# Performance work log

Measured on AMD Instinct MI355X. Metric: run time of the kernel, lower is better.

The kernel has to match this reference:

```python
import jax, jax.numpy as jnp
import numpy as np

B, S, H = 2, 2048, 1024
E, I, IS, K = 16, 512, 2048, 4


def setup_inputs() -> dict:
    key = jax.random.key(0)
    ks = jax.random.split(key, 8)
    s = 0.02
    return {
        "hidden_states": jax.random.normal(ks[0], (B, S, H), jnp.float32),
        "router_w": jax.random.normal(ks[1], (E, H), jnp.float32) * s,
        "gate_up_proj": jax.random.normal(ks[2], (E, 2 * I, H), jnp.float32) * s,
        "down_proj": jax.random.normal(ks[3], (E, H, I), jnp.float32) * s,
        "shared_gate_w": jax.random.normal(ks[4], (IS, H), jnp.float32) * s,
        "shared_up_w": jax.random.normal(ks[5], (IS, H), jnp.float32) * s,
        "shared_down_w": jax.random.normal(ks[6], (H, IS), jnp.float32) * s,
        "shared_expert_gate_w": jax.random.normal(ks[7], (1, H), jnp.float32) * s,
        "top_k": K,
    }


def reference(hidden_states, router_w, gate_up_proj, down_proj,
              shared_gate_w, shared_up_w, shared_down_w,
              shared_expert_gate_w, top_k):
    b, s, h_dim = hidden_states.shape
    N = b * s
    num_experts = router_w.shape[0]
    h = hidden_states.reshape(N, h_dim)

    # ---- shared expert (SwiGLU MLP) ----
    shared_out = (jax.nn.silu(h @ shared_gate_w.T) * (h @ shared_up_w.T)) @ shared_down_w.T
    shared_out = jax.nn.sigmoid(h @ shared_expert_gate_w.T) * shared_out  # [N, H]

    # ---- router: softmax -> top-k -> renormalize ----
    router_logits = h @ router_w.T  # [N, E]
    router_probs_f32 = jax.nn.softmax(router_logits.astype(jnp.float32), axis=-1)
    top_v, top_i = jax.lax.top_k(router_probs_f32, top_k)  # [N, K]
    top_v = top_v / jnp.sum(top_v, axis=-1, keepdims=True)
    top_v = top_v.astype(router_logits.dtype)

    # combine weights scattered to dense [N, E] (zero for unselected experts)
    one_hot = jax.nn.one_hot(top_i, num_experts, dtype=top_v.dtype)  # [N, K, E]
    combine = jnp.sum(one_hot * top_v[..., None], axis=1)  # [N, E]

    # ---- experts: dense dispatch, masked combine (same math as gather/scatter loop) ----
    gu = jnp.einsum('nh,eih->nei', h, gate_up_proj)  # [N, E, 2I]
    gate, up = jnp.split(gu, 2, axis=-1)
    act = jax.nn.silu(gate) * up  # [N, E, I]
    expert_out = jnp.einsum('nei,ehi,ne->nh', act, down_proj, combine)  # [N, H]

    out = expert_out + shared_out

    # ---- aux load-balancing loss (faithful to source, including its reductions) ----
    tokens_per_expert = jnp.sum(one_hot.astype(jnp.float32), axis=(0, 1))  # [E]
    fraction_tokens = tokens_per_expert / (N * top_k)
    router_probs_sum = jnp.sum(jax.nn.softmax(router_logits, axis=-1), axis=0)  # [E]
    fraction_probs = jnp.sum(router_probs_sum) / N  # scalar (as in source)
    aux_loss = num_experts * jnp.sum(fraction_tokens * fraction_probs)

    return out.reshape(b, s, h_dim), aux_loss
```

## Files before the change

### kernel.cpp

```cpp
#include <hip/hip_runtime.h>

typedef __bf16 bf16_t;
typedef bf16_t bf16x4v __attribute__((ext_vector_type(4)));
typedef bf16_t bf16x8v __attribute__((ext_vector_type(8)));
typedef float f32x4 __attribute__((ext_vector_type(4)));

__device__ __forceinline__ void gl_lds16(const void* g, void* l) {
  __builtin_amdgcn_global_load_lds((__attribute__((address_space(1))) void*)g,
                                   (__attribute__((address_space(3))) void*)l,
                                   16, 0, 0);
}

__device__ __forceinline__ float fast_silu(float x) {
  return x / (1.f + __expf(-x));
}

__global__ void cvt_f32_bf16_kernel(const float* __restrict__ in,
                                    bf16_t* __restrict__ out, int n4) {
  int i = blockIdx.x * blockDim.x + threadIdx.x;
  const int stride = gridDim.x * blockDim.x;
  const float4* in4 = (const float4*)in;
  bf16x4v* out4 = (bf16x4v*)out;
  for (; i < n4; i += stride) {
    float4 v = in4[i];
    bf16x4v o;
    o[0] = (bf16_t)v.x; o[1] = (bf16_t)v.y; o[2] = (bf16_t)v.z; o[3] = (bf16_t)v.w;
    out4[i] = o;
  }
}

__global__ __launch_bounds__(256)
void router_topk_kernel(const float* __restrict__ h, const float* __restrict__ rw,
                        const float* __restrict__ segw, float* __restrict__ gsig,
                        int* __restrict__ tokTopI, float* __restrict__ tokTopW) {
  const int t = threadIdx.x;
  const int lane = t & 63;
  const int wid = t >> 6;
  const int grp = lane >> 4;
  const int e = lane & 15;
  const int tok = blockIdx.x * 16 + wid * 4 + grp;

  const float4* h4 = (const float4*)(h + (size_t)tok * 1024);
  const float4* rw4 = (const float4*)(rw + (size_t)e * 1024);
  const float4* sg4 = (const float4*)segw;

  float s = 0.f, ss = 0.f;
  #pragma unroll 8
  for (int c = 0; c < 256; ++c) {
    float4 hv = h4[c];
    float4 wv = rw4[c];
    s += hv.x * wv.x + hv.y * wv.y + hv.z * wv.z + hv.w * wv.w;
    if ((c & 15) == e) {
      float4 gv = sg4[c];
      ss += hv.x * gv.x + hv.y * gv.y + hv.z * gv.z + hv.w * gv.w;
    }
  }
  #pragma unroll
  for (int m = 1; m <= 8; m <<= 1) ss += __shfl_xor(ss, m);
  float mx = s;
  #pragma unroll
  for (int m = 1; m <= 8; m <<= 1) mx = fmaxf(mx, __shfl_xor(mx, m));
  float p = expf(s - mx);

  float pc = p;
  float tsum = 0.f;
  float myw = 0.f; int myi = 0;
  #pragma unroll
  for (int r = 0; r < 4; ++r) {
    float v = pc; int idx = e;
    #pragma unroll
    for (int m = 1; m <= 8; m <<= 1) {
      float ov = __shfl_xor(v, m); int oi = __shfl_xor(idx, m);
      if (ov > v || (ov == v && oi < idx)) { v = ov; idx = oi; }
    }
    tsum += v;
    if (e == r) { myi = idx; myw = v; }
    if (e == idx) pc = -1.f;
  }
  if (e < 4) {
    tokTopI[tok * 4 + e] = myi;
    tokTopW[tok * 4 + e] = myw / tsum;
  }
  if (e == 0) gsig[tok] = 1.f / (1.f + expf(-ss));
}

__global__ __launch_bounds__(256)
void build_lists_kernel(const int* __restrict__ tokTopI,
                        const float* __restrict__ tokTopW,
                        int* __restrict__ cnt, int* __restrict__ toklist,
                        float* __restrict__ wlist) {
  const int e = blockIdx.x;
  const int t = threadIdx.x;
  const int lane = t & 63;
  const int wid = t >> 6;
  __shared__ int base;
  __shared__ int wsum[4];
  if (t == 0) base = 0;
  __syncthreads();

  for (int chunk = 0; chunk < 16; ++chunk) {
    const int i0 = chunk * 1024 + t * 4;
    int4 ti = *(const int4*)&tokTopI[i0];
    const bool f0 = ti.x == e, f1 = ti.y == e, f2 = ti.z == e, f3 = ti.w == e;
    const int c = (int)f0 + (int)f1 + (int)f2 + (int)f3;
    int inc = c;
    #pragma unroll
    for (int m = 1; m <= 32; m <<= 1) {
      int o = __shfl_up(inc, m);
      if (lane >= m) inc += o;
    }
    const int lanePre = inc - c;
    if (lane == 63) wsum[wid] = inc;
    __syncthreads();
    int wavePre = 0;
    #pragma unroll
    for (int w = 0; w < 4; ++w) if (w < wid) wavePre += wsum[w];
    const int total = wsum[0] + wsum[1] + wsum[2] + wsum[3];
    int pos = base + wavePre + lanePre;
    __syncthreads();
    if (t == 0) base += total;
    float4 tw = *(const float4*)&tokTopW[i0];
    if (f0) { toklist[e * 4096 + pos] = i0 >> 2;       wlist[e * 4096 + pos] = tw.x; pos++; }
    if (f1) { toklist[e * 4096 + pos] = (i0 + 1) >> 2; wlist[e * 4096 + pos] = tw.y; pos++; }
    if (f2) { toklist[e * 4096 + pos] = (i0 + 2) >> 2; wlist[e * 4096 + pos] = tw.z; pos++; }
    if (f3) { toklist[e * 4096 + pos] = (i0 + 3) >> 2; wlist[e * 4096 + pos] = tw.w; pos++; }
  }
  __syncthreads();
  if (t == 0) cnt[e] = base;
}

__global__ void finalize_router_kernel(const int* __restrict__ cnt,
                                       int* __restrict__ baseOff,
                                       float* __restrict__ aux) {
  if (threadIdx.x == 0 && blockIdx.x == 0) {
    int s = 0;
    for (int e = 0; e < 16; ++e) { baseOff[e] = s; s += cnt[e]; }
    aux[0] = 16.0f;
  }
}

template<bool GATHER>
__global__ __launch_bounds__(256, 2)
void gateup_gemm_kernel(const bf16_t* __restrict__ A,
                        const bf16_t* __restrict__ B1,
                        const bf16_t* __restrict__ B2,
                        size_t strideBe,
                        bf16_t* __restrict__ actOut, int ldAct,
                        int K, int Mfixed,
                        const int* __restrict__ cnt,
                        const int* __restrict__ baseOff,
                        const int* __restrict__ toklist) {
  const int e = blockIdx.z;
  const int rowBlk = blockIdx.y, colBlk = blockIdx.x;
  int M, actRowBase;
  if constexpr (GATHER) {
    M = cnt[e];
    if (rowBlk * 128 >= M) return;
    actRowBase = baseOff[e] + rowBlk * 128;
  } else {
    M = Mfixed;
    actRowBase = rowBlk * 128;
  }
  const bf16_t* b1 = B1 + (size_t)e * strideBe;
  const bf16_t* b2 = B2 + (size_t)e * strideBe;

  __shared__ __align__(16) bf16_t As[128 * 64];
  __shared__ __align__(16) bf16_t Bs[128 * 64];

  const int t = threadIdx.x;

  const bf16_t* aSrc[4];
  const bf16_t* bSrc[4];
  #pragma unroll
  for (int i = 0; i < 4; ++i) {
    int r = (t >> 3) + 32 * i;
    int grow;
    if constexpr (GATHER) {
      int rr = rowBlk * 128 + r;
      grow = (rr < M) ? toklist[e * 4096 + rr] : 0;
    } else {
      grow = rowBlk * 128 + r;
    }
    aSrc[i] = A + (size_t)grow * K + (t & 7) * 8;
    int j = colBlk * 64 + (r >> 1);
    bSrc[i] = ((r & 1) ? b2 : b1) + (size_t)j * K + (t & 7) * 8;
  }

  f32x4 acc[4][4];
  #pragma unroll
  for (int a = 0; a < 4; ++a)
    #pragma unroll
    for (int b = 0; b < 4; ++b)
      acc[a][b] = (f32x4){0.f, 0.f, 0.f, 0.f};

  const int lane = t & 63;
  const int wid = t >> 6;
  const int wm = wid >> 1, wn = wid & 1;
  const int lr = lane & 15;
  const int lk = (lane >> 4) * 8;

  bf16_t* aDst = As + t * 8;
  bf16_t* bDst = Bs + t * 8;

  for (int k0 = 0; k0 < K; k0 += 64) {
    #pragma unroll
    for (int i = 0; i < 4; ++i) gl_lds16(aSrc[i], aDst + i * 2048);
    #pragma unroll
    for (int i = 0; i < 4; ++i) gl_lds16(bSrc[i], bDst + i * 2048);
    #pragma unroll
    for (int i = 0; i < 4; ++i) { aSrc[i] += 64; bSrc[i] += 64; }
    __syncthreads();
    #pragma unroll
    for (int kk = 0; kk < 64; kk += 32) {
      bf16x8v af[4], bfr[4];
      #pragma unroll
      for (int f = 0; f < 4; ++f)
        af[f] = *(const bf16x8v*)&As[(wm * 64 + f * 16 + lr) * 64 + kk + lk];
      #pragma unroll
      for (int f = 0; f < 4; ++f)
        bfr[f] = *(const bf16x8v*)&Bs[(wn * 64 + f * 16 + lr) * 64 + kk + lk];
      #pragma unroll
      for (int fm = 0; fm < 4; ++fm)
        #pragma unroll
        for (int fn = 0; fn < 4; ++fn)
          acc[fm][fn] = __builtin_amdgcn_mfma_f32_16x16x32_bf16(
              af[fm], bfr[fn], acc[fm][fn], 0, 0, 0);
    }
    __syncthreads();
  }

  const int mRem = M - rowBlk * 128;
  #pragma unroll
  for (int fm = 0; fm < 4; ++fm) {
    #pragma unroll
    for (int fn = 0; fn < 4; ++fn) {
      const int nloc = wn * 64 + fn * 16 + lr;
      const int j = colBlk * 64 + (nloc >> 1);
      const bool even = (nloc & 1) == 0;
      #pragma unroll
      for (int r = 0; r < 4; ++r) {
        float mine = acc[fm][fn][r];
        float other = __shfl_xor(mine, 1);
        float gate = even ? mine : other;
        float up = even ? other : mine;
        float act = fast_silu(gate) * up;
        int tr = wm * 64 + fm * 16 + (lane >> 4) * 4 + r;
        if (even && tr < mRem)
          actOut[(size_t)(actRowBase + tr) * ldAct + j] = (bf16_t)act;
      }
    }
  }
}

template<bool EXPERT>
__global__ __launch_bounds__(256, 2)
void down_gemm_kernel(const bf16_t* __restrict__ Abase,
                      const bf16_t* __restrict__ Bbase,
                      size_t strideBe,
                      float* __restrict__ out,
                      const float* __restrict__ gsig,
                      int K, int Mfixed,
                      const int* __restrict__ cnt,
                      const int* __restrict__ baseOff,
                      const int* __restrict__ toklist,
                      const float* __restrict__ wlist) {
  const int e = blockIdx.z;
  const int rowBlk = blockIdx.y, colBlk = blockIdx.x;
  int M;
  const bf16_t* A;
  if constexpr (EXPERT) {
    M = cnt[e];
    if (rowBlk * 128 >= M) return;
    A = Abase + (size_t)baseOff[e] * K;
  } else {
    M = Mfixed;
    A = Abase;
  }
  const bf16_t* B = Bbase + (size_t)e * strideBe;

  __shared__ __align__(16) bf16_t As[128 * 64];
  __shared__ __align__(16) bf16_t Bs[128 * 64];

  const int t = threadIdx.x;
  const bf16_t* aSrc[4];
  const bf16_t* bSrc[4];
  #pragma unroll
  for (int i = 0; i < 4; ++i) {
    int r = (t >> 3) + 32 * i;
    aSrc[i] = A + (size_t)(rowBlk * 128 + r) * K + (t & 7) * 8;
    bSrc[i] = B + (size_t)(colBlk * 128 + r) * K + (t & 7) * 8;
  }

  f32x4 acc[4][4];
  #pragma unroll
  for (int a = 0; a < 4; ++a)
    #pragma unroll
    for (int b = 0; b < 4; ++b)
      acc[a][b] = (f32x4){0.f, 0.f, 0.f, 0.f};

  const int lane = t & 63;
  const int wid = t >> 6;
  const int wm = wid >> 1, wn = wid & 1;
  const int lr = lane & 15;
  const int lk = (lane >> 4) * 8;

  bf16_t* aDst = As + t * 8;
  bf16_t* bDst = Bs + t * 8;

  for (int k0 = 0; k0 < K; k0 += 64) {
    #pragma unroll
    for (int i = 0; i < 4; ++i) gl_lds16(aSrc[i], aDst + i * 2048);
    #pragma unroll
    for (int i = 0; i < 4; ++i) gl_lds16(bSrc[i], bDst + i * 2048);
    #pragma unroll
    for (int i = 0; i < 4; ++i) { aSrc[i] += 64; bSrc[i] += 64; }
    __syncthreads();
    #pragma unroll
    for (int kk = 0; kk < 64; kk += 32) {
      bf16x8v af[4], bfr[4];
      #pragma unroll
      for (int f = 0; f < 4; ++f)
        af[f] = *(const bf16x8v*)&As[(wm * 64 + f * 16 + lr) * 64 + kk + lk];
      #pragma unroll
      for (int f = 0; f < 4; ++f)
        bfr[f] = *(const bf16x8v*)&Bs[(wn * 64 + f * 16 + lr) * 64 + kk + lk];
      #pragma unroll
      for (int fm = 0; fm < 4; ++fm)
        #pragma unroll
        for (int fn = 0; fn < 4; ++fn)
          acc[fm][fn] = __builtin_amdgcn_mfma_f32_16x16x32_bf16(
              af[fm], bfr[fn], acc[fm][fn], 0, 0, 0);
    }
    __syncthreads();
  }

  const int mRem = M - rowBlk * 128;
  #pragma unroll
  for (int fm = 0; fm < 4; ++fm) {
    #pragma unroll
    for (int r = 0; r < 4; ++r) {
      const int tr = wm * 64 + fm * 16 + (lane >> 4) * 4 + r;
      if (tr < mRem) {
        int tok; float wgt;
        if constexpr (EXPERT) {
          int slot = e * 4096 + rowBlk * 128 + tr;
          tok = toklist[slot];
          wgt = wlist[slot];
        } else {
          tok = rowBlk * 128 + tr;
          wgt = gsig[tok];
        }
        float* orow = out + (size_t)tok * 1024;
        #pragma unroll
        for (int fn = 0; fn < 4; ++fn) {
          const int col = colBlk * 128 + wn * 64 + fn * 16 + lr;
          float v = acc[fm][fn][r] * wgt;
          if constexpr (EXPERT) atomicAdd(orow + col, v);
          else orow[col] = v;
        }
      }
    }
  }
}


extern "C" void kernel_launch(void* const* d_in, const int* in_sizes, int n_in,
                              void* d_out, int out_size, void* d_ws, size_t ws_size,
                              hipStream_t stream) {
  const float* h_f32 = (const float*)d_in[0];
  const float* rw    = (const float*)d_in[1];
  const float* gup   = (const float*)d_in[2];
  const float* dwn   = (const float*)d_in[3];
  const float* sgate = (const float*)d_in[4];
  const float* sup   = (const float*)d_in[5];
  const float* sdown = (const float*)d_in[6];
  const float* segw  = (const float*)d_in[7];

  char* ws = (char*)d_ws;
  bf16_t* h_bf    = (bf16_t*)(ws + 0);
  bf16_t* gup_bf  = (bf16_t*)(ws + 8388608);
  bf16_t* dwn_bf  = (bf16_t*)(ws + 41943040);
  bf16_t* sg_bf   = (bf16_t*)(ws + 58720256);
  bf16_t* su_bf   = (bf16_t*)(ws + 62914560);
  bf16_t* sd_bf   = (bf16_t*)(ws + 67108864);
  bf16_t* act_s   = (bf16_t*)(ws + 71303168);
  bf16_t* act_e   = (bf16_t*)(ws + 88080384);
  float*  gsig    = (float*)(ws + 105119744);
  int*    cnt     = (int*)(ws + 105136128);
  int*    baseOff = (int*)(ws + 105136384);
  int*    toklist = (int*)(ws + 105136640);
  float*  wlist   = (float*)(ws + 105398784);
  int*    tokTopI = (int*)(ws + 105660928);
  float*  tokTopW = (float*)(ws + 105726464);

  float* out = (float*)d_out;
  float* aux = out + 4194304;

  auto cvtLaunch = [&](const float* src, bf16_t* dst, int n) {
    int n4 = n / 4;
    int blocks = (n4 + 255) / 256;
    if (blocks > 2048) blocks = 2048;
    cvt_f32_bf16_kernel<<<blocks, 256, 0, stream>>>(src, dst, n4);
  };
  cvtLaunch(h_f32, h_bf, 4194304);
  cvtLaunch(gup,   gup_bf, 16777216);
  cvtLaunch(dwn,   dwn_bf, 8388608);
  cvtLaunch(sgate, sg_bf, 2097152);
  cvtLaunch(sup,   su_bf, 2097152);
  cvtLaunch(sdown, sd_bf, 2097152);

  router_topk_kernel<<<256, 256, 0, stream>>>(h_f32, rw, segw, gsig, tokTopI, tokTopW);
  build_lists_kernel<<<16, 256, 0, stream>>>(tokTopI, tokTopW, cnt, toklist, wlist);
  finalize_router_kernel<<<1, 64, 0, stream>>>(cnt, baseOff, aux);

  gateup_gemm_kernel<false><<<dim3(32, 32, 1), 256, 0, stream>>>(
      h_bf, sg_bf, su_bf, (size_t)0, act_s, 2048, 1024, 4096,
      nullptr, nullptr, nullptr);
  gateup_gemm_kernel<true><<<dim3(8, 32, 16), 256, 0, stream>>>(
      h_bf, gup_bf, gup_bf + 512 * 1024, (size_t)1024 * 1024, act_e, 512, 1024, 0,
      cnt, baseOff, toklist);
  down_gemm_kernel<false><<<dim3(8, 32, 1), 256, 0, stream>>>(
      act_s, sd_bf, (size_t)0, out, gsig, 2048, 4096,
      nullptr, nullptr, nullptr, nullptr);
  down_gemm_kernel<true><<<dim3(8, 32, 16), 256, 0, stream>>>(
      act_e, dwn_bf, (size_t)1024 * 512, out, nullptr, 512, 0,
      cnt, baseOff, toklist, wlist);
}
```

Before: 509.0 us.

## Replace expert atomic scatter with bf16 staging and combine kernel; swizzle LDS

The expert down-projection now writes weighted results as bf16 rows into a contiguous staging buffer instead of doing fp32 atomicAdd scatter into the output. A new combine kernel then gathers each token's four expert rows through a position map and adds them to the shared-expert output. Both GEMM kernels also XOR-swizzle their LDS tile layout to avoid bank conflicts, and launch bounds now request four blocks per SM. This removes atomic contention, but it adds an extra kernel pass, rounds expert partial outputs to bf16, and reuses the converted gate_up weight buffer as scratch after the gate/up GEMM has finished.

```diff
diff --git a/kernel.cpp b/kernel.cpp
--- a/kernel.cpp
+++ b/kernel.cpp
@@ -88,7 +88,7 @@
 void build_lists_kernel(const int* __restrict__ tokTopI,
                         const float* __restrict__ tokTopW,
                         int* __restrict__ cnt, int* __restrict__ toklist,
-                        float* __restrict__ wlist) {
+                        float* __restrict__ wlist, int* __restrict__ posOf) {
   const int e = blockIdx.x;
   const int t = threadIdx.x;
   const int lane = t & 63;
@@ -120,10 +120,10 @@
     __syncthreads();
     if (t == 0) base += total;
     float4 tw = *(const float4*)&tokTopW[i0];
-    if (f0) { toklist[e * 4096 + pos] = i0 >> 2;       wlist[e * 4096 + pos] = tw.x; pos++; }
-    if (f1) { toklist[e * 4096 + pos] = (i0 + 1) >> 2; wlist[e * 4096 + pos] = tw.y; pos++; }
-    if (f2) { toklist[e * 4096 + pos] = (i0 + 2) >> 2; wlist[e * 4096 + pos] = tw.z; pos++; }
-    if (f3) { toklist[e * 4096 + pos] = (i0 + 3) >> 2; wlist[e * 4096 + pos] = tw.w; pos++; }
+    if (f0) { toklist[e * 4096 + pos] = i0 >> 2;       wlist[e * 4096 + pos] = tw.x; posOf[i0]     = pos; pos++; }
+    if (f1) { toklist[e * 4096 + pos] = (i0 + 1) >> 2; wlist[e * 4096 + pos] = tw.y; posOf[i0 + 1] = pos; pos++; }
+    if (f2) { toklist[e * 4096 + pos] = (i0 + 2) >> 2; wlist[e * 4096 + pos] = tw.z; posOf[i0 + 2] = pos; pos++; }
+    if (f3) { toklist[e * 4096 + pos] = (i0 + 3) >> 2; wlist[e * 4096 + pos] = tw.w; posOf[i0 + 3] = pos; pos++; }
   }
   __syncthreads();
   if (t == 0) cnt[e] = base;
@@ -140,7 +140,7 @@
 }
 
 template<bool GATHER>
-__global__ __launch_bounds__(256, 2)
+__global__ __launch_bounds__(256, 4)
 void gateup_gemm_kernel(const bf16_t* __restrict__ A,
                         const bf16_t* __restrict__ B1,
                         const bf16_t* __restrict__ B2,
@@ -168,6 +168,7 @@
   __shared__ __align__(16) bf16_t Bs[128 * 64];
 
   const int t = threadIdx.x;
+  const int sc = (((t & 7) ^ ((t >> 3) & 7))) * 8;
 
   const bf16_t* aSrc[4];
   const bf16_t* bSrc[4];
@@ -181,9 +182,9 @@
     } else {
       grow = rowBlk * 128 + r;
     }
-    aSrc[i] = A + (size_t)grow * K + (t & 7) * 8;
+    aSrc[i] = A + (size_t)grow * K + sc;
     int j = colBlk * 64 + (r >> 1);
-    bSrc[i] = ((r & 1) ? b2 : b1) + (size_t)j * K + (t & 7) * 8;
+    bSrc[i] = ((r & 1) ? b2 : b1) + (size_t)j * K + sc;
   }
 
   f32x4 acc[4][4];
@@ -214,11 +215,15 @@
     for (int kk = 0; kk < 64; kk += 32) {
       bf16x8v af[4], bfr[4];
       #pragma unroll
-      for (int f = 0; f < 4; ++f)
-        af[f] = *(const bf16x8v*)&As[(wm * 64 + f * 16 + lr) * 64 + kk + lk];
-      #pragma unroll
-      for (int f = 0; f < 4; ++f)
-        bfr[f] = *(const bf16x8v*)&Bs[(wn * 64 + f * 16 + lr) * 64 + kk + lk];
+      for (int f = 0; f < 4; ++f) {
+        const int row = wm * 64 + f * 16 + lr;
+        af[f] = *(const bf16x8v*)&As[row * 64 + ((kk + lk) ^ ((row & 7) << 3))];
+      }
+      #pragma unroll
+      for (int f = 0; f < 4; ++f) {
+        const int row = wn * 64 + f * 16 + lr;
+        bfr[f] = *(const bf16x8v*)&Bs[row * 64 + ((kk + lk) ^ ((row & 7) << 3))];
+      }
       #pragma unroll
       for (int fm = 0; fm < 4; ++fm)
         #pragma unroll
@@ -253,27 +258,29 @@
 }
 
 template<bool EXPERT>
-__global__ __launch_bounds__(256, 2)
+__global__ __launch_bounds__(256, 4)
 void down_gemm_kernel(const bf16_t* __restrict__ Abase,
                       const bf16_t* __restrict__ Bbase,
                       size_t strideBe,
-                      float* __restrict__ out,
+                      float* __restrict__ outF,
+                      bf16_t* __restrict__ outB,
                       const float* __restrict__ gsig,
                       int K, int Mfixed,
                       const int* __restrict__ cnt,
                       const int* __restrict__ baseOff,
-                      const int* __restrict__ toklist,
                       const float* __restrict__ wlist) {
   const int e = blockIdx.z;
   const int rowBlk = blockIdx.y, colBlk = blockIdx.x;
-  int M;
+  int M, aRowBase;
   const bf16_t* A;
   if constexpr (EXPERT) {
     M = cnt[e];
     if (rowBlk * 128 >= M) return;
+    aRowBase = baseOff[e] + rowBlk * 128;
     A = Abase + (size_t)baseOff[e] * K;
   } else {
     M = Mfixed;
+    aRowBase = rowBlk * 128;
     A = Abase;
   }
   const bf16_t* B = Bbase + (size_t)e * strideBe;
@@ -282,13 +289,14 @@
   __shared__ __align__(16) bf16_t Bs[128 * 64];
 
   const int t = threadIdx.x;
+  const int sc = (((t & 7) ^ ((t >> 3) & 7))) * 8;
   const bf16_t* aSrc[4];
   const bf16_t* bSrc[4];
   #pragma unroll
   for (int i = 0; i < 4; ++i) {
     int r = (t >> 3) + 32 * i;
-    aSrc[i] = A + (size_t)(rowBlk * 128 + r) * K + (t & 7) * 8;
-    bSrc[i] = B + (size_t)(colBlk * 128 + r) * K + (t & 7) * 8;
+    aSrc[i] = A + (size_t)(rowBlk * 128 + r) * K + sc;
+    bSrc[i] = B + (size_t)(colBlk * 128 + r) * K + sc;
   }
 
   f32x4 acc[4][4];
@@ -319,11 +327,15 @@
     for (int kk = 0; kk < 64; kk += 32) {
       bf16x8v af[4], bfr[4];
       #pragma unroll
-      for (int f = 0; f < 4; ++f)
-        af[f] = *(const bf16x8v*)&As[(wm * 64 + f * 16 + lr) * 64 + kk + lk];
-      #pragma unroll
-      for (int f = 0; f < 4; ++f)
-        bfr[f] = *(const bf16x8v*)&Bs[(wn * 64 + f * 16 + lr) * 64 + kk + lk];
+      for (int f = 0; f < 4; ++f) {
+        const int row = wm * 64 + f * 16 + lr;
+        af[f] = *(const bf16x8v*)&As[row * 64 + ((kk + lk) ^ ((row & 7) << 3))];
+      }
+      #pragma unroll
+      for (int f = 0; f < 4; ++f) {
+        const int row = wn * 64 + f * 16 + lr;
+        bfr[f] = *(const bf16x8v*)&Bs[row * 64 + ((kk + lk) ^ ((row & 7) << 3))];
+      }
       #pragma unroll
       for (int fm = 0; fm < 4; ++fm)
         #pragma unroll
@@ -341,26 +353,45 @@
     for (int r = 0; r < 4; ++r) {
       const int tr = wm * 64 + fm * 16 + (lane >> 4) * 4 + r;
       if (tr < mRem) {
-        int tok; float wgt;
-        if constexpr (EXPERT) {
-          int slot = e * 4096 + rowBlk * 128 + tr;
-          tok = toklist[slot];
-          wgt = wlist[slot];
-        } else {
-          tok = rowBlk * 128 + tr;
-          wgt = gsig[tok];
-        }
-        float* orow = out + (size_t)tok * 1024;
+        float wgt;
+        if constexpr (EXPERT) wgt = wlist[e * 4096 + rowBlk * 128 + tr];
+        else                  wgt = gsig[rowBlk * 128 + tr];
         #pragma unroll
         for (int fn = 0; fn < 4; ++fn) {
           const int col = colBlk * 128 + wn * 64 + fn * 16 + lr;
           float v = acc[fm][fn][r] * wgt;
-          if constexpr (EXPERT) atomicAdd(orow + col, v);
-          else orow[col] = v;
+          if constexpr (EXPERT)
+            outB[(size_t)(aRowBase + tr) * 1024 + col] = (bf16_t)v;
+          else
+            outF[(size_t)(aRowBase + tr) * 1024 + col] = v;
         }
       }
     }
   }
+}
+
+__global__ __launch_bounds__(256)
+void combine_kernel(const bf16_t* __restrict__ dsc,
+                    const int* __restrict__ tokTopI,
+                    const int* __restrict__ posOf,
+                    const int* __restrict__ baseOff,
+                    float* __restrict__ out) {
+  const int tok = blockIdx.x;
+  const int t = threadIdx.x;
+  __shared__ const bf16_t* rows[4];
+  if (t < 4) {
+    int e = tokTopI[tok * 4 + t];
+    rows[t] = dsc + (size_t)(baseOff[e] + posOf[tok * 4 + t]) * 1024;
+  }
+  __syncthreads();
+  float4* orow = (float4*)(out + (size_t)tok * 1024);
+  float4 v = orow[t];
+  #pragma unroll
+  for (int k = 0; k < 4; ++k) {
+    bf16x4v b = *(const bf16x4v*)(rows[k] + t * 4);
+    v.x += (float)b[0]; v.y += (float)b[1]; v.z += (float)b[2]; v.w += (float)b[3];
+  }
+  orow[t] = v;
 }
 
 
@@ -392,6 +423,8 @@
   float*  wlist   = (float*)(ws + 105398784);
   int*    tokTopI = (int*)(ws + 105660928);
   float*  tokTopW = (float*)(ws + 105726464);
+  int*    posOf   = (int*)(ws + 105791744);
+  bf16_t* dsc     = gup_bf;
 
   float* out = (float*)d_out;
   float* aux = out + 4194304;
@@ -410,7 +443,7 @@
   cvtLaunch(sdown, sd_bf, 2097152);
 
   router_topk_kernel<<<256, 256, 0, stream>>>(h_f32, rw, segw, gsig, tokTopI, tokTopW);
-  build_lists_kernel<<<16, 256, 0, stream>>>(tokTopI, tokTopW, cnt, toklist, wlist);
+  build_lists_kernel<<<16, 256, 0, stream>>>(tokTopI, tokTopW, cnt, toklist, wlist, posOf);
   finalize_router_kernel<<<1, 64, 0, stream>>>(cnt, baseOff, aux);
 
   gateup_gemm_kernel<false><<<dim3(32, 32, 1), 256, 0, stream>>>(
@@ -420,9 +453,10 @@
       h_bf, gup_bf, gup_bf + 512 * 1024, (size_t)1024 * 1024, act_e, 512, 1024, 0,
       cnt, baseOff, toklist);
   down_gemm_kernel<false><<<dim3(8, 32, 1), 256, 0, stream>>>(
-      act_s, sd_bf, (size_t)0, out, gsig, 2048, 4096,
-      nullptr, nullptr, nullptr, nullptr);
+      act_s, sd_bf, (size_t)0, out, nullptr, gsig, 2048, 4096,
+      nullptr, nullptr, nullptr);
   down_gemm_kernel<true><<<dim3(8, 32, 16), 256, 0, stream>>>(
-      act_e, dwn_bf, (size_t)1024 * 512, out, nullptr, 512, 0,
-      cnt, baseOff, toklist, wlist);
-}
+      act_e, dwn_bf, (size_t)1024 * 512, nullptr, dsc, nullptr, 512, 0,
+      cnt, baseOff, wlist);
+  combine_kernel<<<4096, 256, 0, stream>>>(dsc, tokTopI, posOf, baseOff, out);
+}
```

New measurement: 459.9 us. 9.6% less time.
